# Optimization experiments

Measured on AMD Instinct MI355X. Metric: run time of the kernel, lower is better.

Reference implementation:

```python
import jax, jax.numpy as jnp
import numpy as np

L, F, LOG_T, NMIN, NMAX = 16, 2, 19, 16, 2048
T = 2 ** LOG_T
N_ROWS = 524288
PRIMES = np.array([1, 2654435761, 805459861], dtype=np.uint32)
# 8 corner offsets of the unit cube, bits (dx, dy, dz)
CORNERS = np.stack(np.meshgrid([0, 1], [0, 1], [0, 1], indexing='ij'), axis=-1).reshape(8, 3)


def setup_inputs() -> dict:
    key = jax.random.key(0)
    k1, k2 = jax.random.split(key)
    x = jax.random.uniform(k1, (N_ROWS, 3), dtype=jnp.float32)  # coords in [0,1)
    hashmap = jax.random.normal(k2, (L, F, T), dtype=jnp.float32) * 1e-2
    growth = np.exp((np.log(NMAX) - np.log(NMIN)) / (L - 1))
    resolution = jnp.asarray(np.floor(NMIN * growth ** np.arange(L)), dtype=jnp.float32)
    return {"x": x, "hashmap": hashmap, "resolution": resolution}


def _hash_encode(x, hashmap, resolution):
    # x: [n, 3], hashmap: [L, F, T], resolution: [L]
    n = x.shape[0]
    xs = x[:, None, :] * resolution[None, :, None]          # [n, L, 3]
    x0f = jnp.floor(xs)
    frac = xs - x0f                                          # trilinear fracs [n, L, 3]
    x0 = x0f.astype(jnp.uint32)

    primes = jnp.asarray(PRIMES)                             # [3] uint32
    h0 = x0 * primes                                         # [n, L, 3] (wraps mod 2^32)
    h1 = (x0 + jnp.uint32(1)) * primes                       # [n, L, 3]
    hpair = jnp.stack([h0, h1], axis=-2)                     # [n, L, 2, 3]

    c = jnp.asarray(CORNERS, dtype=jnp.int32)                # [8, 3]
    # hashed index per corner: xor of per-dim hashes, masked to table size
    idx = (hpair[:, :, c[:, 0], 0]
           ^ hpair[:, :, c[:, 1], 1]
           ^ hpair[:, :, c[:, 2], 2]) & jnp.uint32(T - 1)    # [n, L, 8]

    wpair = jnp.stack([1.0 - frac, frac], axis=-2)           # [n, L, 2, 3]
    w = (wpair[:, :, c[:, 0], 0]
         * wpair[:, :, c[:, 1], 1]
         * wpair[:, :, c[:, 2], 2])                          # [n, L, 8]

    def per_level(hm_l, idx_l, w_l):
        # hm_l: [F, T], idx_l: [n, 8], w_l: [n, 8]
        feats = jnp.take(hm_l, idx_l, axis=1)                # [F, n, 8]
        return jnp.einsum('fnc,nc->nf', feats, w_l)          # [n, F]

    out = jax.vmap(per_level)(hashmap,
                              idx.transpose(1, 0, 2),
                              w.transpose(1, 0, 2))          # [L, n, F]
    # match torch layout: (L,F,n) -> (n, L, F) -> (n, L*F)
    return out.transpose(1, 0, 2).reshape(n, L * F)


def reference(x, hashmap, resolution):
    return _hash_encode(x, hashmap, resolution)
```

## Files before the change

kernel.cpp:

```cpp
#include <hip/hip_runtime.h>
#include <hip/hip_fp16.h>


#define HG_L     16
#define HG_LOG_T 19
#define HG_T     (1u << HG_LOG_T)
#define HG_N     524288u
#define HP1      2654435761u
#define HP2      805459861u

#define DS0 17u
#define DS1 23u
#define DS2 31u
#define DS3 43u
#define DS4 59u
#define DS5 81u
#define DOFF0 0u
#define DOFF1 4913u
#define DOFF2 17080u
#define DOFF3 46871u
#define DOFF4 126378u
#define DOFF5 331757u
#define DTOTAL 863198u

#define TAB_BYTES ((size_t)HG_L * HG_T * 4u)

__global__ __launch_bounds__(256) void interleave_fp16(
    const float* __restrict__ hm,
    __half2* __restrict__ ws)
{
    const unsigned u = 6u * HG_T + (blockIdx.x * 256u + threadIdx.x) * 4u;
    const unsigned l = u >> HG_LOG_T;
    const unsigned t = u & (HG_T - 1u);
    const float* base = hm + (size_t)l * (2u * HG_T);
    const float4 a = *reinterpret_cast<const float4*>(base + t);
    const float4 b = *reinterpret_cast<const float4*>(base + HG_T + t);
    __half2 h0 = __floats2half2_rn(a.x, b.x);
    __half2 h1 = __floats2half2_rn(a.y, b.y);
    __half2 h2 = __floats2half2_rn(a.z, b.z);
    __half2 h3 = __floats2half2_rn(a.w, b.w);
    uint4 o;
    o.x = *reinterpret_cast<unsigned*>(&h0);
    o.y = *reinterpret_cast<unsigned*>(&h1);
    o.z = *reinterpret_cast<unsigned*>(&h2);
    o.w = *reinterpret_cast<unsigned*>(&h3);
    *reinterpret_cast<uint4*>(ws + u) = o;
}

__device__ __forceinline__ unsigned pack_h2(float f0, float f1) {
    __half2 h = __floats2half2_rn(f0, f1);
    return *reinterpret_cast<unsigned*>(&h);
}

__global__ __launch_bounds__(256) void build_quad(
    const float* __restrict__ hm,
    uint4* __restrict__ quad)
{
    const unsigned l = blockIdx.y;
    unsigned S, off;
    switch (l) {
        case 0: S = DS0; off = DOFF0; break;
        case 1: S = DS1; off = DOFF1; break;
        case 2: S = DS2; off = DOFF2; break;
        case 3: S = DS3; off = DOFF3; break;
        case 4: S = DS4; off = DOFF4; break;
        default: S = DS5; off = DOFF5; break;
    }
    const unsigned i = blockIdx.x * 256u + threadIdx.x;
    if (i >= S * S * S) return;
    const unsigned x  = i % S;
    const unsigned t1 = i / S;
    const unsigned y  = t1 % S;
    const unsigned z  = t1 / S;
    const unsigned M = HG_T - 1u;
    const unsigned hz = z * HP2;
    const unsigned hy0 = y * HP1, hy1 = hy0 + HP1;
    const unsigned i00 = (hy0 ^ hz ^ x) & M;
    const unsigned i10 = (hy0 ^ hz ^ (x + 1u)) & M;
    const unsigned i01 = (hy1 ^ hz ^ x) & M;
    const unsigned i11 = (hy1 ^ hz ^ (x + 1u)) & M;
    const float* b0 = hm + (size_t)l * (2u * HG_T);
    uint4 o;
    o.x = pack_h2(b0[i00], b0[i00 + HG_T]);
    o.y = pack_h2(b0[i10], b0[i10 + HG_T]);
    o.z = pack_h2(b0[i01], b0[i01 + HG_T]);
    o.w = pack_h2(b0[i11], b0[i11 + HG_T]);
    quad[off + i] = o;
}

__device__ __forceinline__ float2 hfv(unsigned raw) {
    return __half22float2(*reinterpret_cast<const __half2*>(&raw));
}

template <unsigned S, unsigned OFF>
__device__ __forceinline__ float2 enc_dense(
    float px, float py, float pz, float res,
    const uint4* __restrict__ quad)
{
    const float xs0 = px * res, xs1 = py * res, xs2 = pz * res;
    const float fl0 = floorf(xs0), fl1 = floorf(xs1), fl2 = floorf(xs2);
    const float fr0 = xs0 - fl0, fr1 = xs1 - fl1, fr2 = xs2 - fl2;
    const unsigned x0 = (unsigned)fl0;
    const unsigned y0 = (unsigned)fl1;
    const unsigned z0 = (unsigned)fl2;

    const unsigned i = (z0 * S + y0) * S + x0 + OFF;
    const uint4 q0 = quad[i];
    const uint4 q1 = quad[i + S * S];

    const float w0x = 1.0f - fr0, w1x = fr0;
    const float w0y = 1.0f - fr1, w1y = fr1;
    const float w0z = 1.0f - fr2, w1z = fr2;

    const float2 a00 = hfv(q0.x), a10 = hfv(q0.y), a01 = hfv(q0.z), a11 = hfv(q0.w);
    const float2 b00 = hfv(q1.x), b10 = hfv(q1.y), b01 = hfv(q1.z), b11 = hfv(q1.w);

    const float s0x = w0y * (w0x * a00.x + w1x * a10.x) + w1y * (w0x * a01.x + w1x * a11.x);
    const float s0y = w0y * (w0x * a00.y + w1x * a10.y) + w1y * (w0x * a01.y + w1x * a11.y);
    const float s1x = w0y * (w0x * b00.x + w1x * b10.x) + w1y * (w0x * b01.x + w1x * b11.x);
    const float s1y = w0y * (w0x * b00.y + w1x * b10.y) + w1y * (w0x * b01.y + w1x * b11.y);

    return make_float2(w0z * s0x + w1z * s1x, w0z * s0y + w1z * s1y);
}

__device__ __forceinline__ float2 enc_hash(
    float px, float py, float pz, float res,
    const uint2* __restrict__ tab2)
{
    const float xs0 = px * res, xs1 = py * res, xs2 = pz * res;
    const float fl0 = floorf(xs0), fl1 = floorf(xs1), fl2 = floorf(xs2);
    const float fr0 = xs0 - fl0, fr1 = xs1 - fl1, fr2 = xs2 - fl2;
    const unsigned x0 = (unsigned)fl0;
    const unsigned y0 = (unsigned)fl1;
    const unsigned z0 = (unsigned)fl2;
    const unsigned M = HG_T - 1u;

    const unsigned hy0 = y0 * HP1, hy1 = hy0 + HP1;
    const unsigned hz0 = z0 * HP2, hz1 = hz0 + HP2;
    const unsigned H0 = hy0 ^ hz0;
    const unsigned H1 = hy1 ^ hz0;
    const unsigned H2 = hy0 ^ hz1;
    const unsigned H3 = hy1 ^ hz1;

    unsigned r0[4], r1[4];
    {
        const unsigned i0 = (H0 ^ x0) & M; const uint2 q = tab2[i0 >> 1];
        r0[0] = (i0 & 1u) ? q.y : q.x;  r1[0] = (i0 & 1u) ? q.x : q.y;
    }
    {
        const unsigned i0 = (H1 ^ x0) & M; const uint2 q = tab2[i0 >> 1];
        r0[1] = (i0 & 1u) ? q.y : q.x;  r1[1] = (i0 & 1u) ? q.x : q.y;
    }
    {
        const unsigned i0 = (H2 ^ x0) & M; const uint2 q = tab2[i0 >> 1];
        r0[2] = (i0 & 1u) ? q.y : q.x;  r1[2] = (i0 & 1u) ? q.x : q.y;
    }
    {
        const unsigned i0 = (H3 ^ x0) & M; const uint2 q = tab2[i0 >> 1];
        r0[3] = (i0 & 1u) ? q.y : q.x;  r1[3] = (i0 & 1u) ? q.x : q.y;
    }
    if (x0 & 1u) {
        const unsigned xp = x0 + 1u;
        { const unsigned i1 = (H0 ^ xp) & M; const uint2 q = tab2[i1 >> 1];
          r1[0] = (i1 & 1u) ? q.y : q.x; }
        { const unsigned i1 = (H1 ^ xp) & M; const uint2 q = tab2[i1 >> 1];
          r1[1] = (i1 & 1u) ? q.y : q.x; }
        { const unsigned i1 = (H2 ^ xp) & M; const uint2 q = tab2[i1 >> 1];
          r1[2] = (i1 & 1u) ? q.y : q.x; }
        { const unsigned i1 = (H3 ^ xp) & M; const uint2 q = tab2[i1 >> 1];
          r1[3] = (i1 & 1u) ? q.y : q.x; }
    }

    const float w0x = 1.0f - fr0, w1x = fr0;
    const float w00 = (1.0f - fr1) * (1.0f - fr2);
    const float w10 = fr1 * (1.0f - fr2);
    const float w01 = (1.0f - fr1) * fr2;
    const float w11 = fr1 * fr2;

    float ax = 0.0f, ay = 0.0f;
    { const float2 v0 = hfv(r0[0]), v1 = hfv(r1[0]);
      ax += w00 * (w0x * v0.x + w1x * v1.x);
      ay += w00 * (w0x * v0.y + w1x * v1.y); }
    { const float2 v0 = hfv(r0[1]), v1 = hfv(r1[1]);
      ax += w10 * (w0x * v0.x + w1x * v1.x);
      ay += w10 * (w0x * v0.y + w1x * v1.y); }
    { const float2 v0 = hfv(r0[2]), v1 = hfv(r1[2]);
      ax += w01 * (w0x * v0.x + w1x * v1.x);
      ay += w01 * (w0x * v0.y + w1x * v1.y); }
    { const float2 v0 = hfv(r0[3]), v1 = hfv(r1[3]);
      ax += w11 * (w0x * v0.x + w1x * v1.x);
      ay += w11 * (w0x * v0.y + w1x * v1.y); }
    return make_float2(ax, ay);
}

__global__ __launch_bounds__(256) void hg_main(
    const float* __restrict__ x,
    const uint2* __restrict__ tab2,
    const uint4* __restrict__ quad,
    const float* __restrict__ resolution,
    float*       __restrict__ out)
{
    const unsigned tid = threadIdx.x;
    const unsigned p0  = blockIdx.x * 512u + tid;
    const unsigned p1  = p0 + 256u;

    const float ax0 = x[p0 * 3 + 0], ay0 = x[p0 * 3 + 1], az0 = x[p0 * 3 + 2];
    const float ax1 = x[p1 * 3 + 0], ay1 = x[p1 * 3 + 1], az1 = x[p1 * 3 + 2];

    {
        float2 A0[8], A1[8];
        A0[0] = enc_dense<DS0, DOFF0>(ax0, ay0, az0, resolution[0], quad);
        A1[0] = enc_dense<DS0, DOFF0>(ax1, ay1, az1, resolution[0], quad);
        A0[1] = enc_dense<DS1, DOFF1>(ax0, ay0, az0, resolution[1], quad);
        A1[1] = enc_dense<DS1, DOFF1>(ax1, ay1, az1, resolution[1], quad);
        A0[2] = enc_dense<DS2, DOFF2>(ax0, ay0, az0, resolution[2], quad);
        A1[2] = enc_dense<DS2, DOFF2>(ax1, ay1, az1, resolution[2], quad);
        A0[3] = enc_dense<DS3, DOFF3>(ax0, ay0, az0, resolution[3], quad);
        A1[3] = enc_dense<DS3, DOFF3>(ax1, ay1, az1, resolution[3], quad);
        A0[4] = enc_dense<DS4, DOFF4>(ax0, ay0, az0, resolution[4], quad);
        A1[4] = enc_dense<DS4, DOFF4>(ax1, ay1, az1, resolution[4], quad);
        A0[5] = enc_dense<DS5, DOFF5>(ax0, ay0, az0, resolution[5], quad);
        A1[5] = enc_dense<DS5, DOFF5>(ax1, ay1, az1, resolution[5], quad);
#pragma unroll
        for (int l = 6; l < 8; ++l) {
            const float res = resolution[l];
            const uint2* tl = tab2 + (size_t)l * (HG_T / 2u);
            A0[l] = enc_hash(ax0, ay0, az0, res, tl);
            A1[l] = enc_hash(ax1, ay1, az1, res, tl);
        }
        float4* d0 = reinterpret_cast<float4*>(out + (size_t)p0 * 32u);
        float4* d1 = reinterpret_cast<float4*>(out + (size_t)p1 * 32u);
        d0[0] = make_float4(A0[0].x, A0[0].y, A0[1].x, A0[1].y);
        d0[1] = make_float4(A0[2].x, A0[2].y, A0[3].x, A0[3].y);
        d0[2] = make_float4(A0[4].x, A0[4].y, A0[5].x, A0[5].y);
        d0[3] = make_float4(A0[6].x, A0[6].y, A0[7].x, A0[7].y);
        d1[0] = make_float4(A1[0].x, A1[0].y, A1[1].x, A1[1].y);
        d1[1] = make_float4(A1[2].x, A1[2].y, A1[3].x, A1[3].y);
        d1[2] = make_float4(A1[4].x, A1[4].y, A1[5].x, A1[5].y);
        d1[3] = make_float4(A1[6].x, A1[6].y, A1[7].x, A1[7].y);
    }
    {
        float2 A0[8], A1[8];
#pragma unroll
        for (int l = 8; l < 16; ++l) {
            const float res = resolution[l];
            const uint2* tl = tab2 + (size_t)l * (HG_T / 2u);
            A0[l - 8] = enc_hash(ax0, ay0, az0, res, tl);
            A1[l - 8] = enc_hash(ax1, ay1, az1, res, tl);
        }
        float4* d0 = reinterpret_cast<float4*>(out + (size_t)p0 * 32u + 16u);
        float4* d1 = reinterpret_cast<float4*>(out + (size_t)p1 * 32u + 16u);
        d0[0] = make_float4(A0[0].x, A0[0].y, A0[1].x, A0[1].y);
        d0[1] = make_float4(A0[2].x, A0[2].y, A0[3].x, A0[3].y);
        d0[2] = make_float4(A0[4].x, A0[4].y, A0[5].x, A0[5].y);
        d0[3] = make_float4(A0[6].x, A0[6].y, A0[7].x, A0[7].y);
        d1[0] = make_float4(A1[0].x, A1[0].y, A1[1].x, A1[1].y);
        d1[1] = make_float4(A1[2].x, A1[2].y, A1[3].x, A1[3].y);
        d1[2] = make_float4(A1[4].x, A1[4].y, A1[5].x, A1[5].y);
        d1[3] = make_float4(A1[6].x, A1[6].y, A1[7].x, A1[7].y);
    }
}

extern "C" void kernel_launch(void* const* d_in, const int* in_sizes, int n_in,
                              void* d_out, int out_size, void* d_ws, size_t ws_size,
                              hipStream_t stream) {
    const float* x          = (const float*)d_in[0];
    const float* hashmap    = (const float*)d_in[1];
    const float* resolution = (const float*)d_in[2];
    float* out              = (float*)d_out;

    __half2* wst  = (__half2*)d_ws;
    uint4*   quad = (uint4*)((char*)d_ws + TAB_BYTES);

    hipLaunchKernelGGL(interleave_fp16,
                       dim3((10u * HG_T / 4u) / 256u), dim3(256), 0, stream,
                       hashmap, wst);
    hipLaunchKernelGGL(build_quad,
                       dim3((DS5 * DS5 * DS5 + 255u) / 256u, 6), dim3(256), 0, stream,
                       hashmap, quad);

    hipLaunchKernelGGL(hg_main, dim3(HG_N / 512u), dim3(256), 0, stream,
                       x, (const uint2*)d_ws, quad, resolution, out);
}
```

Before: 338.3 us.

## Merge prep kernels and split main encoder into low and high level kernels

Fuses the fp16 interleave and dense-quad build into one prep launch that dispatches on block index, and packs the dense tables linearly without idle blocks. The main encoder is split into two kernels, one for levels 0-7 (dense plus two hash levels) and one for levels 8-15, each handling one point per thread with launch-bound occupancy hints. The aim is lower register pressure, higher occupancy for latency-bound gathers, and a better L2 working set per kernel. The cost is reading x twice and an extra launch, and the 64-byte output rows are now written in two separate passes.

```diff
diff --git a/kernel.cpp b/kernel.cpp
--- a/kernel.cpp
+++ b/kernel.cpp
@@ -25,49 +25,45 @@
 
 #define TAB_BYTES ((size_t)HG_L * HG_T * 4u)
 
-__global__ __launch_bounds__(256) void interleave_fp16(
-    const float* __restrict__ hm,
-    __half2* __restrict__ ws)
-{
-    const unsigned u = 6u * HG_T + (blockIdx.x * 256u + threadIdx.x) * 4u;
-    const unsigned l = u >> HG_LOG_T;
-    const unsigned t = u & (HG_T - 1u);
-    const float* base = hm + (size_t)l * (2u * HG_T);
-    const float4 a = *reinterpret_cast<const float4*>(base + t);
-    const float4 b = *reinterpret_cast<const float4*>(base + HG_T + t);
-    __half2 h0 = __floats2half2_rn(a.x, b.x);
-    __half2 h1 = __floats2half2_rn(a.y, b.y);
-    __half2 h2 = __floats2half2_rn(a.z, b.z);
-    __half2 h3 = __floats2half2_rn(a.w, b.w);
-    uint4 o;
-    o.x = *reinterpret_cast<unsigned*>(&h0);
-    o.y = *reinterpret_cast<unsigned*>(&h1);
-    o.z = *reinterpret_cast<unsigned*>(&h2);
-    o.w = *reinterpret_cast<unsigned*>(&h3);
-    *reinterpret_cast<uint4*>(ws + u) = o;
-}
+#define NB_INTER 5120u
+#define NB_QUAD  3372u
 
 __device__ __forceinline__ unsigned pack_h2(float f0, float f1) {
     __half2 h = __floats2half2_rn(f0, f1);
     return *reinterpret_cast<unsigned*>(&h);
 }
 
-__global__ __launch_bounds__(256) void build_quad(
+__global__ __launch_bounds__(256) void hg_prep(
     const float* __restrict__ hm,
+    __half2* __restrict__ wst,
     uint4* __restrict__ quad)
 {
-    const unsigned l = blockIdx.y;
-    unsigned S, off;
-    switch (l) {
-        case 0: S = DS0; off = DOFF0; break;
-        case 1: S = DS1; off = DOFF1; break;
-        case 2: S = DS2; off = DOFF2; break;
-        case 3: S = DS3; off = DOFF3; break;
-        case 4: S = DS4; off = DOFF4; break;
-        default: S = DS5; off = DOFF5; break;
-    }
-    const unsigned i = blockIdx.x * 256u + threadIdx.x;
-    if (i >= S * S * S) return;
+    const unsigned bid = blockIdx.x;
+    if (bid < NB_INTER) {
+        const unsigned u = 6u * HG_T + (bid * 256u + threadIdx.x) * 4u;
+        const unsigned l = u >> HG_LOG_T;
+        const unsigned t = u & (HG_T - 1u);
+        const float* base = hm + (size_t)l * (2u * HG_T);
+        const float4 a = *reinterpret_cast<const float4*>(base + t);
+        const float4 b = *reinterpret_cast<const float4*>(base + HG_T + t);
+        uint4 o;
+        o.x = pack_h2(a.x, b.x);
+        o.y = pack_h2(a.y, b.y);
+        o.z = pack_h2(a.z, b.z);
+        o.w = pack_h2(a.w, b.w);
+        *reinterpret_cast<uint4*>(wst + u) = o;
+        return;
+    }
+    const unsigned j = (bid - NB_INTER) * 256u + threadIdx.x;
+    if (j >= DTOTAL) return;
+    unsigned l, S, off;
+    if      (j < DOFF1) { l = 0; S = DS0; off = DOFF0; }
+    else if (j < DOFF2) { l = 1; S = DS1; off = DOFF1; }
+    else if (j < DOFF3) { l = 2; S = DS2; off = DOFF2; }
+    else if (j < DOFF4) { l = 3; S = DS3; off = DOFF3; }
+    else if (j < DOFF5) { l = 4; S = DS4; off = DOFF4; }
+    else                { l = 5; S = DS5; off = DOFF5; }
+    const unsigned i  = j - off;
     const unsigned x  = i % S;
     const unsigned t1 = i / S;
     const unsigned y  = t1 % S;
@@ -85,7 +81,7 @@
     o.y = pack_h2(b0[i10], b0[i10 + HG_T]);
     o.z = pack_h2(b0[i01], b0[i01 + HG_T]);
     o.w = pack_h2(b0[i11], b0[i11 + HG_T]);
-    quad[off + i] = o;
+    quad[j] = o;
 }
 
 __device__ __forceinline__ float2 hfv(unsigned raw) {
@@ -193,71 +189,55 @@
     return make_float2(ax, ay);
 }
 
-__global__ __launch_bounds__(256) void hg_main(
+__global__ __launch_bounds__(256, 8) void hg_lo(
     const float* __restrict__ x,
     const uint2* __restrict__ tab2,
     const uint4* __restrict__ quad,
     const float* __restrict__ resolution,
     float*       __restrict__ out)
 {
-    const unsigned tid = threadIdx.x;
-    const unsigned p0  = blockIdx.x * 512u + tid;
-    const unsigned p1  = p0 + 256u;
-
-    const float ax0 = x[p0 * 3 + 0], ay0 = x[p0 * 3 + 1], az0 = x[p0 * 3 + 2];
-    const float ax1 = x[p1 * 3 + 0], ay1 = x[p1 * 3 + 1], az1 = x[p1 * 3 + 2];
-
-    {
-        float2 A0[8], A1[8];
-        A0[0] = enc_dense<DS0, DOFF0>(ax0, ay0, az0, resolution[0], quad);
-        A1[0] = enc_dense<DS0, DOFF0>(ax1, ay1, az1, resolution[0], quad);
-        A0[1] = enc_dense<DS1, DOFF1>(ax0, ay0, az0, resolution[1], quad);
-        A1[1] = enc_dense<DS1, DOFF1>(ax1, ay1, az1, resolution[1], quad);
-        A0[2] = enc_dense<DS2, DOFF2>(ax0, ay0, az0, resolution[2], quad);
-        A1[2] = enc_dense<DS2, DOFF2>(ax1, ay1, az1, resolution[2], quad);
-        A0[3] = enc_dense<DS3, DOFF3>(ax0, ay0, az0, resolution[3], quad);
-        A1[3] = enc_dense<DS3, DOFF3>(ax1, ay1, az1, resolution[3], quad);
-        A0[4] = enc_dense<DS4, DOFF4>(ax0, ay0, az0, resolution[4], quad);
-        A1[4] = enc_dense<DS4, DOFF4>(ax1, ay1, az1, resolution[4], quad);
-        A0[5] = enc_dense<DS5, DOFF5>(ax0, ay0, az0, resolution[5], quad);
-        A1[5] = enc_dense<DS5, DOFF5>(ax1, ay1, az1, resolution[5], quad);
+    const unsigned p = blockIdx.x * 256u + threadIdx.x;
+    const float ax = x[p * 3 + 0], ay = x[p * 3 + 1], az = x[p * 3 + 2];
+    float4* d = reinterpret_cast<float4*>(out + (size_t)p * 32u);
+    {
+        const float2 a = enc_dense<DS0, DOFF0>(ax, ay, az, resolution[0], quad);
+        const float2 b = enc_dense<DS1, DOFF1>(ax, ay, az, resolution[1], quad);
+        d[0] = make_float4(a.x, a.y, b.x, b.y);
+    }
+    {
+        const float2 a = enc_dense<DS2, DOFF2>(ax, ay, az, resolution[2], quad);
+        const float2 b = enc_dense<DS3, DOFF3>(ax, ay, az, resolution[3], quad);
+        d[1] = make_float4(a.x, a.y, b.x, b.y);
+    }
+    {
+        const float2 a = enc_dense<DS4, DOFF4>(ax, ay, az, resolution[4], quad);
+        const float2 b = enc_dense<DS5, DOFF5>(ax, ay, az, resolution[5], quad);
+        d[2] = make_float4(a.x, a.y, b.x, b.y);
+    }
+    {
+        const float2 a = enc_hash(ax, ay, az, resolution[6], tab2 + 6u * (HG_T / 2u));
+        const float2 b = enc_hash(ax, ay, az, resolution[7], tab2 + 7u * (HG_T / 2u));
+        d[3] = make_float4(a.x, a.y, b.x, b.y);
+    }
+}
+
+__global__ __launch_bounds__(256, 6) void hg_hi(
+    const float* __restrict__ x,
+    const uint2* __restrict__ tab2,
+    const float* __restrict__ resolution,
+    float*       __restrict__ out)
+{
+    const unsigned p = blockIdx.x * 256u + threadIdx.x;
+    const float ax = x[p * 3 + 0], ay = x[p * 3 + 1], az = x[p * 3 + 2];
+    float4* d = reinterpret_cast<float4*>(out + (size_t)p * 32u + 16u);
 #pragma unroll
-        for (int l = 6; l < 8; ++l) {
-            const float res = resolution[l];
-            const uint2* tl = tab2 + (size_t)l * (HG_T / 2u);
-            A0[l] = enc_hash(ax0, ay0, az0, res, tl);
-            A1[l] = enc_hash(ax1, ay1, az1, res, tl);
-        }
-        float4* d0 = reinterpret_cast<float4*>(out + (size_t)p0 * 32u);
-        float4* d1 = reinterpret_cast<float4*>(out + (size_t)p1 * 32u);
-        d0[0] = make_float4(A0[0].x, A0[0].y, A0[1].x, A0[1].y);
-        d0[1] = make_float4(A0[2].x, A0[2].y, A0[3].x, A0[3].y);
-        d0[2] = make_float4(A0[4].x, A0[4].y, A0[5].x, A0[5].y);
-        d0[3] = make_float4(A0[6].x, A0[6].y, A0[7].x, A0[7].y);
-        d1[0] = make_float4(A1[0].x, A1[0].y, A1[1].x, A1[1].y);
-        d1[1] = make_float4(A1[2].x, A1[2].y, A1[3].x, A1[3].y);
-        d1[2] = make_float4(A1[4].x, A1[4].y, A1[5].x, A1[5].y);
-        d1[3] = make_float4(A1[6].x, A1[6].y, A1[7].x, A1[7].y);
-    }
-    {
-        float2 A0[8], A1[8];
-#pragma unroll
-        for (int l = 8; l < 16; ++l) {
-            const float res = resolution[l];
-            const uint2* tl = tab2 + (size_t)l * (HG_T / 2u);
-            A0[l - 8] = enc_hash(ax0, ay0, az0, res, tl);
-            A1[l - 8] = enc_hash(ax1, ay1, az1, res, tl);
-        }
-        float4* d0 = reinterpret_cast<float4*>(out + (size_t)p0 * 32u + 16u);
-        float4* d1 = reinterpret_cast<float4*>(out + (size_t)p1 * 32u + 16u);
-        d0[0] = make_float4(A0[0].x, A0[0].y, A0[1].x, A0[1].y);
-        d0[1] = make_float4(A0[2].x, A0[2].y, A0[3].x, A0[3].y);
-        d0[2] = make_float4(A0[4].x, A0[4].y, A0[5].x, A0[5].y);
-        d0[3] = make_float4(A0[6].x, A0[6].y, A0[7].x, A0[7].y);
-        d1[0] = make_float4(A1[0].x, A1[0].y, A1[1].x, A1[1].y);
-        d1[1] = make_float4(A1[2].x, A1[2].y, A1[3].x, A1[3].y);
-        d1[2] = make_float4(A1[4].x, A1[4].y, A1[5].x, A1[5].y);
-        d1[3] = make_float4(A1[6].x, A1[6].y, A1[7].x, A1[7].y);
+    for (int pr = 0; pr < 4; ++pr) {
+        const int l0 = 8 + 2 * pr;
+        const float2 a = enc_hash(ax, ay, az, resolution[l0],
+                                  tab2 + (size_t)l0 * (HG_T / 2u));
+        const float2 b = enc_hash(ax, ay, az, resolution[l0 + 1],
+                                  tab2 + (size_t)(l0 + 1) * (HG_T / 2u));
+        d[pr] = make_float4(a.x, a.y, b.x, b.y);
     }
 }
 
@@ -272,13 +252,11 @@
     __half2* wst  = (__half2*)d_ws;
     uint4*   quad = (uint4*)((char*)d_ws + TAB_BYTES);
 
-    hipLaunchKernelGGL(interleave_fp16,
-                       dim3((10u * HG_T / 4u) / 256u), dim3(256), 0, stream,
-                       hashmap, wst);
-    hipLaunchKernelGGL(build_quad,
-                       dim3((DS5 * DS5 * DS5 + 255u) / 256u, 6), dim3(256), 0, stream,
-                       hashmap, quad);
-
-    hipLaunchKernelGGL(hg_main, dim3(HG_N / 512u), dim3(256), 0, stream,
+    hipLaunchKernelGGL(hg_prep, dim3(NB_INTER + NB_QUAD), dim3(256), 0, stream,
+                       hashmap, wst, quad);
+
+    hipLaunchKernelGGL(hg_lo, dim3(HG_N / 256u), dim3(256), 0, stream,
                        x, (const uint2*)d_ws, quad, resolution, out);
-}
+    hipLaunchKernelGGL(hg_hi, dim3(HG_N / 256u), dim3(256), 0, stream,
+                       x, (const uint2*)d_ws, resolution, out);
+}
```

After: 456.6 us. 1.35x slower.
